# Performance work log

Hardware: AMD Instinct MI355X
Metric: run time of the kernel (lower is better)

## Reference

```python
import jax, jax.numpy as jnp
import numpy as np
import math

SIDE = 48          # image height = width (positions = SIDE*SIDE)
WIN = 3            # window_size (odd, image mode)
K = WIN * WIN      # neighbor_count
FD = 32            # field_dim
HID = 64           # hidden_dim
NH = 4             # num_hypotheses
RD = 8             # relative_dim
JOINT = 3 * FD + RD
CLIP = 3.0
TEMP = 1.0
GATE_EPS = 1e-6
ETA = 1.0          # warmup_eta


def _neighbor_windows(x, side, win):
    B = x.shape[0]
    rest = x.shape[2:]
    g = x.reshape((B, side, side) + rest)
    p = win // 2
    gp = jnp.pad(g, [(0, 0), (p, p), (p, p)] + [(0, 0)] * len(rest))
    w = jnp.stack([gp[:, dy:dy + side, dx:dx + side]
                   for dy in range(win) for dx in range(win)], axis=3)
    return w.reshape((B, side * side, win * win) + rest)


def _mlp(x, w1, b1, w2, b2):
    # Linear -> GELU (exact, like torch nn.GELU()) -> Linear, squeeze last dim
    return (jax.nn.gelu(x @ w1 + b1, approximate=False) @ w2 + b2)[..., 0]


def setup_inputs() -> dict:
    key = jax.random.key(0)
    ks = jax.random.split(key, 16)
    B, P = 2, SIDE * SIDE
    inp = {
        'hypothesis_state': jax.random.normal(ks[0], (B, P, NH, FD), jnp.float32),
        'activation': jax.random.uniform(ks[1], (B, P, NH), jnp.float32),
        'drive': jax.random.uniform(ks[2], (B, P, NH), jnp.float32),
        'resistance': jax.random.uniform(ks[3], (B, P, NH), jnp.float32),
        'relative': 0.02 * jax.random.normal(ks[4], (K, RD), jnp.float32),
        'ln_w': jnp.ones((JOINT,), jnp.float32),
        'ln_b': jnp.zeros((JOINT,), jnp.float32),
        'sup_w1': jax.random.normal(ks[5], (JOINT, HID), jnp.float32) / math.sqrt(JOINT),
        'sup_b1': jnp.zeros((HID,), jnp.float32),
        'sup_w2': jax.random.normal(ks[6], (HID, 1), jnp.float32) / math.sqrt(HID),
        'sup_b2': jnp.zeros((1,), jnp.float32),
        'con_w1': jax.random.normal(ks[7], (JOINT, HID), jnp.float32) / math.sqrt(JOINT),
        'con_b1': jnp.zeros((HID,), jnp.float32),
        'con_w2': jax.random.normal(ks[8], (HID, 1), jnp.float32) / math.sqrt(HID),
        'con_b2': jnp.zeros((1,), jnp.float32),
        'eml_bias': jnp.float32(-0.1),
    }
    return inp


def reference(hypothesis_state, activation, drive, resistance, relative,
              ln_w, ln_b, sup_w1, sup_b1, sup_w2, sup_b2,
              con_w1, con_b1, con_w2, con_b2, eml_bias):
    B, P, H, D = hypothesis_state.shape
    side = int(math.isqrt(P))
    # windowed neighbor gather (image mode, zero-padded 3x3)
    sw = _neighbor_windows(hypothesis_state, side, WIN)   # [B,P,K,H,D]
    aw = _neighbor_windows(activation, side, WIN)          # [B,P,K,H]
    valid = _neighbor_windows(jnp.ones((1, P), hypothesis_state.dtype), side, WIN)  # [1,P,K]

    shp = (B, P, H, K, H)
    tgt = jnp.broadcast_to(hypothesis_state[:, :, :, None, None, :], shp + (D,))
    src = jnp.broadcast_to(sw[:, :, None, :, :, :], shp + (D,))
    rel = jnp.broadcast_to(relative[None, None, None, :, None, :], shp + (RD,))
    joint = jnp.concatenate([tgt, src, tgt - src, rel], axis=-1)  # [B,P,H,K,H,JOINT]
    mu = joint.mean(-1, keepdims=True)
    var = joint.var(-1, keepdims=True)
    joint = (joint - mu) * jax.lax.rsqrt(var + 1e-5) * ln_w + ln_b

    support_value = jax.nn.softplus(_mlp(joint, sup_w1, sup_b1, sup_w2, sup_b2))  # [B,P,H,K,H]
    conflict_value = jax.nn.softplus(_mlp(joint, con_w1, con_b1, con_w2, con_b2))

    gate = aw[:, :, None, :, :] * valid[:, :, None, :, None]   # [B,P,1,K,H]
    gate_mass = jnp.maximum(gate.sum((3, 4)), GATE_EPS)        # [B,P,1]
    support = (support_value * gate).sum((3, 4)) / gate_mass   # [B,P,H]
    conflict = (conflict_value * gate).sum((3, 4)) / gate_mass

    pdrive = drive + support
    presist = resistance + conflict
    # EMLUnit(dim=1, clip_value, init_bias=-0.1): clipped warmup-scaled drive/resistance balance
    energy = jnp.clip(ETA * (pdrive - presist) + eml_bias, -CLIP, CLIP)
    # EMLActivationBudget(temperature)
    act = jax.nn.sigmoid(energy / TEMP)
    budget_loss = act.mean()
    entropy = -(act * jnp.log(act + 1e-8) + (1.0 - act) * jnp.log(1.0 - act + 1e-8)).mean()
    active_rate = (act > 0.5).astype(jnp.float32).mean()

    return (support, conflict, pdrive, presist, energy, act,
            jnp.broadcast_to(gate_mass, support.shape), budget_loss, entropy, active_rate)
```

## Files before the change

### kernel.cpp

```cpp
#include <hip/hip_runtime.h>
#include <hip/hip_bf16.h>
#include <math.h>

#define SIDE 48
#define PPOS (SIDE*SIDE)
#define NBATCH 2
#define NHYP 4
#define FD 32
#define RD 8
#define NJ 104
#define NBP (NBATCH*PPOS)
#define NOUT (NBP*NHYP)
#define THREADS 512
#define NROWS 576
#define NBLK (NBP/4)
#define WS_SR   16
#define WS_SQR  28
#define WS_SC   40
#define WS_RC   64
#define WS_S    1216
#define WS_T    1344
#define WS_W2   1472
#define WS_WBF  1600
#define WS_WAF  3648
#define WS_PART 5696

typedef __attribute__((ext_vector_type(8))) short short8;
typedef __attribute__((ext_vector_type(4))) float f32x4;
typedef __attribute__((ext_vector_type(2))) float f32x2;
union U8 { uint4 u4; short8 s8; };

__device__ __forceinline__ float bflo(unsigned u) { return __uint_as_float(u << 16); }
__device__ __forceinline__ float bfhi(unsigned u) { return __uint_as_float(u & 0xffff0000u); }
__device__ __forceinline__ unsigned packbf2(float a, float b) {
    unsigned ua = __float_as_uint(a), ub = __float_as_uint(b);
    unsigned ra = (ua + 0x7fffu + ((ua >> 16) & 1u)) >> 16;
    unsigned rb = (ub + 0x7fffu + ((ub >> 16) & 1u)) & 0xffff0000u;
    return ra | rb;
}
__device__ __forceinline__ float softplusf(float v) {
    return fmaxf(v, 0.f) + log1pf(expf(-fabsf(v)));
}

#define W1X(kk, j) ((j) < 64 ? sup_w1[(kk)*64 + (j)] : con_w1[(kk)*64 + (j) - 64])

__global__ __launch_bounds__(512) void eml_fold(
    const float* __restrict__ rel, const float* __restrict__ ln_w, const float* __restrict__ ln_b,
    const float* __restrict__ sup_w1, const float* __restrict__ sup_b1,
    const float* __restrict__ sup_w2, const float* __restrict__ sup_b2,
    const float* __restrict__ con_w1, const float* __restrict__ con_b1,
    const float* __restrict__ con_w2, const float* __restrict__ con_b2,
    const float* __restrict__ eml_bias, float* __restrict__ ws)
{
    const int tid = threadIdx.x;
    const int bid = blockIdx.x;
    unsigned* wsd = reinterpret_cast<unsigned*>(ws);
    __shared__ float pS[4][128], pT[4][128];

    if (bid < 8) {
        int u = bid*512 + tid;
        int sel = u >> 11, v2 = u & 2047;
        int n = v2 >> 8, l = (v2 >> 2) & 63, j = v2 & 3;
        int k0 = (l >> 4)*8 + 2*j, col = n*16 + (l & 15);
        float lo, hi;
        if (sel == 0) {
            lo = ln_w[32+k0]*W1X(32+k0,col)     - ln_w[64+k0]*W1X(64+k0,col);
            hi = ln_w[32+k0+1]*W1X(32+k0+1,col) - ln_w[64+k0+1]*W1X(64+k0+1,col);
        } else {
            lo = ln_w[k0]*W1X(k0,col)     + ln_w[64+k0]*W1X(64+k0,col);
            hi = ln_w[k0+1]*W1X(k0+1,col) + ln_w[64+k0+1]*W1X(64+k0+1,col);
        }
        wsd[(sel ? WS_WAF : WS_WBF) + v2] = packbf2(lo, hi);
    } else if (bid == 8) {
        #pragma unroll
        for (int u0 = 0; u0 < 2; ++u0) {
            int u = u0*512 + tid;
            int k = u >> 7, j = u & 127;
            float a = 0.f;
            #pragma unroll
            for (int i = 0; i < 8; ++i) a += rel[k*8+i] * ln_w[96+i] * W1X(96+i, j);
            ws[WS_RC + u] = a;
        }
    } else if (bid == 9) {
        if (tid < 128) {
            int u = 1024 + tid;
            int k = u >> 7, j = u & 127;
            float a = 0.f;
            #pragma unroll
            for (int i = 0; i < 8; ++i) a += rel[k*8+i] * ln_w[96+i] * W1X(96+i, j);
            ws[WS_RC + u] = a;
        } else if (tid < 137) {
            int kk = tid - 128;
            float s = 0.f, sq = 0.f;
            #pragma unroll
            for (int i = 0; i < 8; ++i) { float v = rel[kk*8+i]; s += v; sq += v*v; }
            ws[WS_SR+kk] = s; ws[WS_SQR+kk] = sq;
        } else if (tid == 140) {
            ws[WS_SC] = sup_b2[0]; ws[WS_SC+1] = con_b2[0]; ws[WS_SC+2] = eml_bias[0];
        }
    } else {
        int col = tid & 127, seg = tid >> 7;
        float S = 0.f, T = 0.f;
        for (int kk = seg*26; kk < seg*26 + 26; ++kk) {
            float w = W1X(kk, col);
            S += ln_w[kk]*w; T += ln_b[kk]*w;
        }
        pS[seg][col] = S; pT[seg][col] = T;
        __syncthreads();
        if (tid < 128) {
            float Tt = pT[0][tid] + pT[1][tid] + pT[2][tid] + pT[3][tid]
                       + (tid < 64 ? sup_b1[tid] : con_b1[tid-64]);
            ws[WS_S + tid]  = pS[0][tid] + pS[1][tid] + pS[2][tid] + pS[3][tid];
            ws[WS_T + tid]  = Tt * 32.f + 512.5f;
            ws[WS_W2 + tid] = (tid < 64 ? sup_w2[tid] : con_w2[tid-64]);
        }
    }
}

__global__ __launch_bounds__(THREADS, 8) void eml_main(
    const float* __restrict__ hs, const float* __restrict__ act_in,
    const float* __restrict__ drive, const float* __restrict__ resist,
    float* __restrict__ out, const float* __restrict__ cst,
    float* __restrict__ part)
{
    __shared__ __align__(16) unsigned sB[64*68];
    __shared__ __align__(16) float    sA[16*132];
    __shared__ union __align__(16) UU {
        __hip_bfloat16 snb[64*40];
        unsigned svcv[NROWS];
    } u;
    __shared__ __align__(16) float sdot[64*16];
    __shared__ __align__(16) float sgelu[1024];
    __shared__ float sact[64], sSt[64], sSq[64];
    __shared__ float sSr[9], sSqr[9];

    const int tid = threadIdx.x;
    const int blk = blockIdx.x;
    const int b   = blk / 576;
    const int rm  = blk % 576;
    const int y0  = (rm / 24) * 2;
    const int x0  = (rm % 24) * 2;

    #pragma unroll
    for (int i = tid; i < 1024; i += THREADS) {
        float x = (float)(i - 512) * 0.03125f;
        sgelu[i] = 0.5f * x * (1.0f + erff(x * 0.70710678118654752f));
    }

    const int vec = tid >> 3, q = tid & 7;
    const int nb1 = vec >> 2, h1 = vec & 3;
    const int yy = y0 + (nb1 >> 2) - 1, xx = x0 + (nb1 & 3) - 1;
    const bool vld = (yy >= 0) && (yy < SIDE) && (xx >= 0) && (xx < SIDE);
    const int npos = b*PPOS + yy*SIDE + xx;
    float4 v = make_float4(0.f, 0.f, 0.f, 0.f);
    if (vld) v = *reinterpret_cast<const float4*>(&hs[((size_t)npos*NHYP + h1)*FD + q*4]);
    {
        unsigned* drow = reinterpret_cast<unsigned*>(&u.snb[vec*40]);
        drow[q*2]   = packbf2(v.x, v.y);
        drow[q*2+1] = packbf2(v.z, v.w);
        float s  = v.x + v.y + v.z + v.w;
        float sq = v.x*v.x + v.y*v.y + v.z*v.z + v.w*v.w;
        s += __shfl_xor(s, 1); sq += __shfl_xor(sq, 1);
        s += __shfl_xor(s, 2); sq += __shfl_xor(sq, 2);
        s += __shfl_xor(s, 4); sq += __shfl_xor(sq, 4);
        if (q == 0) {
            sSt[vec] = s; sSq[vec] = sq;
            sact[vec] = vld ? act_in[npos*NHYP + h1] : 0.f;
        }
    }
    if (tid < 9) { sSr[tid] = cst[WS_SR+tid]; sSqr[tid] = cst[WS_SQR+tid]; }
    __syncthreads();

    {
        const int wv = tid >> 6, lane = tid & 63;
        const int fr = lane & 15, fq = lane >> 4;
        const char* snbB = reinterpret_cast<const char*>(u.snb);
        U8 bB, bA;
        bB.u4 = reinterpret_cast<const uint4*>(cst + WS_WBF)[wv*64 + lane];
        bA.u4 = reinterpret_cast<const uint4*>(cst + WS_WAF)[wv*64 + lane];
        #pragma unroll
        for (int m = 0; m < 4; ++m) {
            U8 a; a.u4 = *reinterpret_cast<const uint4*>(snbB + (m*16 + fr)*80 + fq*16);
            f32x4 acc = {0.f, 0.f, 0.f, 0.f};
            acc = __builtin_amdgcn_mfma_f32_16x16x32_bf16(a.s8, bB.s8, acc, 0, 0, 0);
            #pragma unroll
            for (int j = 0; j < 4; ++j) {
                float o = __shfl_xor(acc[j], 1);
                if (!(lane & 1))
                    sB[(m*16 + fq*4 + j)*68 + wv*8 + (fr >> 1)] = packbf2(acc[j], o);
            }
        }
        const int trow = (fr < 8) ? (20 + fr) : (28 + fr);
        U8 at; at.u4 = *reinterpret_cast<const uint4*>(snbB + trow*80 + fq*16);
        {
            f32x4 acc = {0.f, 0.f, 0.f, 0.f};
            acc = __builtin_amdgcn_mfma_f32_16x16x32_bf16(at.s8, bA.s8, acc, 0, 0, 0);
            #pragma unroll
            for (int j = 0; j < 4; ++j)
                sA[(fq*4 + j)*132 + wv*16 + fr] = acc[j];
        }
        if (wv < 4) {
            U8 s2; s2.u4 = *reinterpret_cast<const uint4*>(snbB + (wv*16 + fr)*80 + fq*16);
            f32x4 acc = {0.f, 0.f, 0.f, 0.f};
            acc = __builtin_amdgcn_mfma_f32_16x16x32_bf16(at.s8, s2.s8, acc, 0, 0, 0);
            *reinterpret_cast<f32x4*>(&sdot[(wv*16 + fr)*16 + fq*4]) = acc;
        }
    }
    __syncthreads();

    for (int ri = tid; ri < NROWS; ri += THREADS) {
        const int pos = ri / 144, r = ri % 144;
        const int hh = r / 36, s = r % 36, k = s >> 2, h2 = s & 3;
        const int nbr  = ((pos >> 1) + k/3)*4 + ((pos & 1) + k%3);
        const int srow = nbr*4 + h2;
        const float gate = sact[srow];
        float svv = 0.f, cvv = 0.f;
        if (gate > 0.f) {
            const int cidx = pos*4 + hh;
            const int crow = (pos < 2 ? 20 : 28) + cidx;
            const float dot = sdot[srow*16 + cidx];
            const float mu   = (2.f*sSt[crow] + sSr[k]) * (1.f/NJ);
            const float ssum = 2.f*sSq[crow] + 2.f*sSq[srow] - 2.f*dot + sSqr[k];
            const float rinv = rsqrtf(ssum*(1.f/NJ) - mu*mu + 1e-5f);
            const float r32  = rinv * 32.f;
            const float b32  = -mu * r32;
            const f32x2 r32_2 = {r32, r32};
            const f32x2 b32_2 = {b32, b32};
            const float* aR  = &sA[cidx*132];
            const uint4* bR  = reinterpret_cast<const uint4*>(&sB[srow*68]);
            const float* rck = cst + WS_RC + k*128;
            const f32x2* S2  = reinterpret_cast<const f32x2*>(cst + WS_S);
            const f32x2* T2  = reinterpret_cast<const f32x2*>(cst + WS_T);
            float outs = 0.f, outc = 0.f;
            #pragma unroll 2
            for (int jq = 0; jq < 16; ++jq) {
                uint4 ub = bR[jq];
                const f32x2* a2 = reinterpret_cast<const f32x2*>(aR + jq*8);
                const f32x2* c2 = reinterpret_cast<const f32x2*>(rck + jq*8);
                float accv = 0.f;
                #define PAIR(UW, P) { \
                    f32x2 bv; bv.x = bflo(UW); bv.y = bfhi(UW); \
                    f32x2 d  = a2[P] + bv + c2[P]; \
                    f32x2 qv = r32_2*d + (b32_2*S2[jq*4+P] + T2[jq*4+P]); \
                    float g0 = sgelu[(unsigned)qv.x]; \
                    float g1 = sgelu[(unsigned)qv.y]; \
                    accv = fmaf(g0, cst[WS_W2 + jq*8 + 2*(P)], accv); \
                    accv = fmaf(g1, cst[WS_W2 + jq*8 + 2*(P) + 1], accv); }
                PAIR(ub.x, 0)
                PAIR(ub.y, 1)
                PAIR(ub.z, 2)
                PAIR(ub.w, 3)
                #undef PAIR
                if (jq < 8) outs += accv; else outc += accv;
            }
            svv = softplusf(outs + cst[WS_SC]);
            cvv = softplusf(outc + cst[WS_SC+1]);
        }
        u.svcv[ri] = packbf2(svv*gate, cvv*gate);
    }
    __syncthreads();

    if (tid < 64) {
        const int pos4 = tid >> 4, hh4 = (tid >> 2) & 3, qq = tid & 3;
        float svs = 0.f, cvs = 0.f, mass = 0.f;
        #pragma unroll
        for (int i = 0; i < 9; ++i) {
            int s = qq*9 + i;
            unsigned pp = u.svcv[pos4*144 + hh4*36 + s];
            svs += bflo(pp); cvs += bfhi(pp);
            int kk = s >> 2, h2 = s & 3;
            int nbr = ((pos4 >> 1) + kk/3)*4 + ((pos4 & 1) + kk%3);
            mass += sact[nbr*4 + h2];
        }
        svs += __shfl_xor(svs, 1); cvs += __shfl_xor(cvs, 1); mass += __shfl_xor(mass, 1);
        svs += __shfl_xor(svs, 2); cvs += __shfl_xor(cvs, 2); mass += __shfl_xor(mass, 2);
        float bl = 0.f, en = 0.f, ar = 0.f;
        if (qq == 0) {
            mass = fmaxf(mass, 1e-6f);
            const float support  = svs / mass;
            const float conflict = cvs / mass;
            const int bph = (b*PPOS + (y0 + (pos4 >> 1))*SIDE + x0 + (pos4 & 1))*NHYP + hh4;
            const float pd = drive[bph]  + support;
            const float pr = resist[bph] + conflict;
            float e = fminf(fmaxf(pd - pr + cst[WS_SC+2], -3.f), 3.f);
            const float a = 1.f / (1.f + expf(-e));
            out[0*NOUT + bph] = support;
            out[1*NOUT + bph] = conflict;
            out[2*NOUT + bph] = pd;
            out[3*NOUT + bph] = pr;
            out[4*NOUT + bph] = e;
            out[5*NOUT + bph] = a;
            out[6*NOUT + bph] = mass;
            bl = a;
            en = -(a*logf(a + 1e-8f) + (1.f - a)*logf(1.f - a + 1e-8f));
            ar = (a > 0.5f) ? 1.f : 0.f;
        }
        #pragma unroll
        for (int off = 32; off > 0; off >>= 1) {
            bl += __shfl_down(bl, off); en += __shfl_down(en, off); ar += __shfl_down(ar, off);
        }
        if (tid == 0) {
            part[blk]          = bl;
            part[NBLK + blk]   = en;
            part[2*NBLK + blk] = ar;
        }
    }
}

__global__ __launch_bounds__(256) void eml_final(const float* __restrict__ part, float* __restrict__ out3)
{
    __shared__ float red[4*3];
    float bl = 0.f, en = 0.f, ar = 0.f;
    for (int i = threadIdx.x; i < NBLK; i += 256) {
        bl += part[i];
        en += part[NBLK + i];
        ar += part[2*NBLK + i];
    }
    #pragma unroll
    for (int off = 32; off > 0; off >>= 1) {
        bl += __shfl_down(bl, off); en += __shfl_down(en, off); ar += __shfl_down(ar, off);
    }
    const int lane = threadIdx.x & 63, wid = threadIdx.x >> 6;
    if (lane == 0) { red[wid*3] = bl; red[wid*3+1] = en; red[wid*3+2] = ar; }
    __syncthreads();
    if (threadIdx.x == 0) {
        float b2 = 0.f, e2 = 0.f, a2 = 0.f;
        for (int w = 0; w < 4; ++w) { b2 += red[w*3]; e2 += red[w*3+1]; a2 += red[w*3+2]; }
        const float inv = 1.0f / (float)NOUT;
        out3[0] = b2*inv; out3[1] = e2*inv; out3[2] = a2*inv;
    }
}

extern "C" void kernel_launch(void* const* d_in, const int* in_sizes, int n_in,
                              void* d_out, int out_size, void* d_ws, size_t ws_size,
                              hipStream_t stream)
{
    (void)in_sizes; (void)n_in; (void)out_size; (void)ws_size;
    const float* hs    = (const float*)d_in[0];
    const float* act   = (const float*)d_in[1];
    const float* drv   = (const float*)d_in[2];
    const float* res   = (const float*)d_in[3];
    const float* rel   = (const float*)d_in[4];
    const float* lnw   = (const float*)d_in[5];
    const float* lnb   = (const float*)d_in[6];
    const float* sw1   = (const float*)d_in[7];
    const float* sb1   = (const float*)d_in[8];
    const float* sw2   = (const float*)d_in[9];
    const float* sb2   = (const float*)d_in[10];
    const float* cw1   = (const float*)d_in[11];
    const float* cb1   = (const float*)d_in[12];
    const float* cw2   = (const float*)d_in[13];
    const float* cb2   = (const float*)d_in[14];
    const float* ebias = (const float*)d_in[15];
    float* out = (float*)d_out;
    float* ws  = (float*)d_ws;

    eml_fold<<<dim3(11), dim3(512), 0, stream>>>(
        rel, lnw, lnb, sw1, sb1, sw2, sb2, cw1, cb1, cw2, cb2, ebias, ws);
    eml_main<<<dim3(NBLK), dim3(THREADS), 0, stream>>>(
        hs, act, drv, res, out, ws, ws + WS_PART);
    eml_final<<<dim3(1), dim3(256), 0, stream>>>(ws + WS_PART, out + 7*NOUT);
}
```

Baseline: 47.64 us.

## Enlarge per-block tile from 2x2 to 2x3 positions to cut halo overhead

Each block now handles a 2x3 patch of output positions, so it loads a 4x5 neighbor halo instead of 2x2 positions with a 4x4 halo. Each loaded neighbor row feeds more outputs, and the grid shrinks from 1152 to 768 blocks. The MFMA tiles for the projections and dot products are reorganised around the 24 center rows, and the final partial reduction now spans two waves through shared memory. In exchange, shared memory per block grows, the occupancy hint drops from 8 to 6, and some MFMA lanes do padded work.

```diff
diff --git a/kernel.cpp b/kernel.cpp
--- a/kernel.cpp
+++ b/kernel.cpp
@@ -12,8 +12,8 @@
 #define NBP (NBATCH*PPOS)
 #define NOUT (NBP*NHYP)
 #define THREADS 512
-#define NROWS 576
-#define NBLK (NBP/4)
+#define NROWS 864
+#define NBLK 768
 #define WS_SR   16
 #define WS_SQR  28
 #define WS_SC   40
@@ -117,29 +117,29 @@
     }
 }
 
-__global__ __launch_bounds__(THREADS, 8) void eml_main(
+__global__ __launch_bounds__(THREADS, 6) void eml_main(
     const float* __restrict__ hs, const float* __restrict__ act_in,
     const float* __restrict__ drive, const float* __restrict__ resist,
     float* __restrict__ out, const float* __restrict__ cst,
     float* __restrict__ part)
 {
-    __shared__ __align__(16) unsigned sB[64*68];
-    __shared__ __align__(16) float    sA[16*132];
+    __shared__ __align__(16) unsigned sB[80*68];
+    __shared__ __align__(16) float    sA[24*132];
     __shared__ union __align__(16) UU {
-        __hip_bfloat16 snb[64*40];
+        __hip_bfloat16 snb[80*40];
         unsigned svcv[NROWS];
     } u;
-    __shared__ __align__(16) float sdot[64*16];
+    __shared__ __align__(16) float sdot[80*24];
     __shared__ __align__(16) float sgelu[1024];
-    __shared__ float sact[64], sSt[64], sSq[64];
+    __shared__ float sact[80], sSt[80], sSq[80];
     __shared__ float sSr[9], sSqr[9];
 
     const int tid = threadIdx.x;
     const int blk = blockIdx.x;
-    const int b   = blk / 576;
-    const int rm  = blk % 576;
-    const int y0  = (rm / 24) * 2;
-    const int x0  = (rm % 24) * 2;
+    const int b   = blk / 384;
+    const int rm  = blk % 384;
+    const int y0  = (rm / 16) * 2;
+    const int x0  = (rm % 16) * 3;
 
     #pragma unroll
     for (int i = tid; i < 1024; i += THREADS) {
@@ -147,22 +147,28 @@
         sgelu[i] = 0.5f * x * (1.0f + erff(x * 0.70710678118654752f));
     }
 
-    const int vec = tid >> 3, q = tid & 7;
-    const int nb1 = vec >> 2, h1 = vec & 3;
-    const int yy = y0 + (nb1 >> 2) - 1, xx = x0 + (nb1 & 3) - 1;
-    const bool vld = (yy >= 0) && (yy < SIDE) && (xx >= 0) && (xx < SIDE);
-    const int npos = b*PPOS + yy*SIDE + xx;
-    float4 v = make_float4(0.f, 0.f, 0.f, 0.f);
-    if (vld) v = *reinterpret_cast<const float4*>(&hs[((size_t)npos*NHYP + h1)*FD + q*4]);
-    {
+    if (tid < 320) {
+        const int vec = tid >> 2, q = tid & 3;
+        const int nb1 = vec >> 2, h1 = vec & 3;
+        const int ny = nb1 / 5, nx = nb1 % 5;
+        const int yy = y0 + ny - 1, xx = x0 + nx - 1;
+        const bool vld = (yy >= 0) && (yy < SIDE) && (xx >= 0) && (xx < SIDE);
+        const int npos = b*PPOS + yy*SIDE + xx;
+        float4 v0 = make_float4(0.f,0.f,0.f,0.f), v1 = make_float4(0.f,0.f,0.f,0.f);
+        if (vld) {
+            const float4* p = reinterpret_cast<const float4*>(&hs[((size_t)npos*NHYP + h1)*FD + q*8]);
+            v0 = p[0]; v1 = p[1];
+        }
         unsigned* drow = reinterpret_cast<unsigned*>(&u.snb[vec*40]);
-        drow[q*2]   = packbf2(v.x, v.y);
-        drow[q*2+1] = packbf2(v.z, v.w);
-        float s  = v.x + v.y + v.z + v.w;
-        float sq = v.x*v.x + v.y*v.y + v.z*v.z + v.w*v.w;
+        drow[q*4+0] = packbf2(v0.x, v0.y);
+        drow[q*4+1] = packbf2(v0.z, v0.w);
+        drow[q*4+2] = packbf2(v1.x, v1.y);
+        drow[q*4+3] = packbf2(v1.z, v1.w);
+        float s  = (v0.x+v0.y+v0.z+v0.w) + (v1.x+v1.y+v1.z+v1.w);
+        float sq = (v0.x*v0.x+v0.y*v0.y+v0.z*v0.z+v0.w*v0.w)
+                 + (v1.x*v1.x+v1.y*v1.y+v1.z*v1.z+v1.w*v1.w);
         s += __shfl_xor(s, 1); sq += __shfl_xor(sq, 1);
         s += __shfl_xor(s, 2); sq += __shfl_xor(sq, 2);
-        s += __shfl_xor(s, 4); sq += __shfl_xor(sq, 4);
         if (q == 0) {
             sSt[vec] = s; sSq[vec] = sq;
             sact[vec] = vld ? act_in[npos*NHYP + h1] : 0.f;
@@ -179,7 +185,7 @@
         bB.u4 = reinterpret_cast<const uint4*>(cst + WS_WBF)[wv*64 + lane];
         bA.u4 = reinterpret_cast<const uint4*>(cst + WS_WAF)[wv*64 + lane];
         #pragma unroll
-        for (int m = 0; m < 4; ++m) {
+        for (int m = 0; m < 5; ++m) {
             U8 a; a.u4 = *reinterpret_cast<const uint4*>(snbB + (m*16 + fr)*80 + fq*16);
             f32x4 acc = {0.f, 0.f, 0.f, 0.f};
             acc = __builtin_amdgcn_mfma_f32_16x16x32_bf16(a.s8, bB.s8, acc, 0, 0, 0);
@@ -190,20 +196,44 @@
                     sB[(m*16 + fq*4 + j)*68 + wv*8 + (fr >> 1)] = packbf2(acc[j], o);
             }
         }
-        const int trow = (fr < 8) ? (20 + fr) : (28 + fr);
-        U8 at; at.u4 = *reinterpret_cast<const uint4*>(snbB + trow*80 + fq*16);
+        const int pos0 = fr >> 2, hh0 = fr & 3;
+        const int trow0 = ((pos0/3 + 1)*5 + (pos0%3) + 1)*4 + hh0;
+        int trow1 = 0;
+        if (fr < 8) {
+            const int t1 = 16 + fr, pos1 = t1 >> 2, hh1 = t1 & 3;
+            trow1 = ((pos1/3 + 1)*5 + (pos1%3) + 1)*4 + hh1;
+        }
+        U8 at0, at1;
+        at0.u4 = *reinterpret_cast<const uint4*>(snbB + trow0*80 + fq*16);
+        at1.u4 = *reinterpret_cast<const uint4*>(snbB + trow1*80 + fq*16);
         {
             f32x4 acc = {0.f, 0.f, 0.f, 0.f};
-            acc = __builtin_amdgcn_mfma_f32_16x16x32_bf16(at.s8, bA.s8, acc, 0, 0, 0);
+            acc = __builtin_amdgcn_mfma_f32_16x16x32_bf16(at0.s8, bA.s8, acc, 0, 0, 0);
             #pragma unroll
             for (int j = 0; j < 4; ++j)
                 sA[(fq*4 + j)*132 + wv*16 + fr] = acc[j];
         }
-        if (wv < 4) {
-            U8 s2; s2.u4 = *reinterpret_cast<const uint4*>(snbB + (wv*16 + fr)*80 + fq*16);
+        {
             f32x4 acc = {0.f, 0.f, 0.f, 0.f};
-            acc = __builtin_amdgcn_mfma_f32_16x16x32_bf16(at.s8, s2.s8, acc, 0, 0, 0);
-            *reinterpret_cast<f32x4*>(&sdot[(wv*16 + fr)*16 + fq*4]) = acc;
+            acc = __builtin_amdgcn_mfma_f32_16x16x32_bf16(at1.s8, bA.s8, acc, 0, 0, 0);
+            if (fq < 2) {
+                #pragma unroll
+                for (int j = 0; j < 4; ++j)
+                    sA[(16 + fq*4 + j)*132 + wv*16 + fr] = acc[j];
+            }
+        }
+        #pragma unroll
+        for (int pass = 0; pass < 2; ++pass) {
+            int uu = pass ? (8 + wv) : wv;
+            if (pass && wv >= 2) break;
+            const int mt = uu / 5, n = uu % 5;
+            U8 sfr; sfr.u4 = *reinterpret_cast<const uint4*>(snbB + (n*16 + fr)*80 + fq*16);
+            f32x4 acc = {0.f, 0.f, 0.f, 0.f};
+            acc = __builtin_amdgcn_mfma_f32_16x16x32_bf16(mt ? at1.s8 : at0.s8, sfr.s8, acc, 0, 0, 0);
+            if (!mt)
+                *reinterpret_cast<f32x4*>(&sdot[(n*16 + fr)*24 + fq*4]) = acc;
+            else if (fq < 2)
+                *reinterpret_cast<f32x4*>(&sdot[(n*16 + fr)*24 + 16 + fq*4]) = acc;
         }
     }
     __syncthreads();
@@ -211,14 +241,15 @@
     for (int ri = tid; ri < NROWS; ri += THREADS) {
         const int pos = ri / 144, r = ri % 144;
         const int hh = r / 36, s = r % 36, k = s >> 2, h2 = s & 3;
-        const int nbr  = ((pos >> 1) + k/3)*4 + ((pos & 1) + k%3);
+        const int py = pos / 3, px = pos % 3;
+        const int nbr  = (py + k/3)*5 + (px + k%3);
         const int srow = nbr*4 + h2;
         const float gate = sact[srow];
         float svv = 0.f, cvv = 0.f;
         if (gate > 0.f) {
             const int cidx = pos*4 + hh;
-            const int crow = (pos < 2 ? 20 : 28) + cidx;
-            const float dot = sdot[srow*16 + cidx];
+            const int crow = ((py + 1)*5 + px + 1)*4 + hh;
+            const float dot = sdot[srow*24 + cidx];
             const float mu   = (2.f*sSt[crow] + sSr[k]) * (1.f/NJ);
             const float ssum = 2.f*sSq[crow] + 2.f*sSq[srow] - 2.f*dot + sSqr[k];
             const float rinv = rsqrtf(ssum*(1.f/NJ) - mu*mu + 1e-5f);
@@ -260,8 +291,11 @@
     }
     __syncthreads();
 
-    if (tid < 64) {
-        const int pos4 = tid >> 4, hh4 = (tid >> 2) & 3, qq = tid & 3;
+    float bl = 0.f, en = 0.f, ar = 0.f;
+    if (tid < 96) {
+        const int g = tid >> 2, qq = tid & 3;
+        const int pos4 = g >> 2, hh4 = g & 3;
+        const int py = pos4 / 3, px = pos4 % 3;
         float svs = 0.f, cvs = 0.f, mass = 0.f;
         #pragma unroll
         for (int i = 0; i < 9; ++i) {
@@ -269,17 +303,16 @@
             unsigned pp = u.svcv[pos4*144 + hh4*36 + s];
             svs += bflo(pp); cvs += bfhi(pp);
             int kk = s >> 2, h2 = s & 3;
-            int nbr = ((pos4 >> 1) + kk/3)*4 + ((pos4 & 1) + kk%3);
+            int nbr = (py + kk/3)*5 + (px + kk%3);
             mass += sact[nbr*4 + h2];
         }
         svs += __shfl_xor(svs, 1); cvs += __shfl_xor(cvs, 1); mass += __shfl_xor(mass, 1);
         svs += __shfl_xor(svs, 2); cvs += __shfl_xor(cvs, 2); mass += __shfl_xor(mass, 2);
-        float bl = 0.f, en = 0.f, ar = 0.f;
         if (qq == 0) {
             mass = fmaxf(mass, 1e-6f);
             const float support  = svs / mass;
             const float conflict = cvs / mass;
-            const int bph = (b*PPOS + (y0 + (pos4 >> 1))*SIDE + x0 + (pos4 & 1))*NHYP + hh4;
+            const int bph = (b*PPOS + (y0 + py)*SIDE + x0 + px)*NHYP + hh4;
             const float pd = drive[bph]  + support;
             const float pr = resist[bph] + conflict;
             float e = fminf(fmaxf(pd - pr + cst[WS_SC+2], -3.f), 3.f);
@@ -295,15 +328,23 @@
             en = -(a*logf(a + 1e-8f) + (1.f - a)*logf(1.f - a + 1e-8f));
             ar = (a > 0.5f) ? 1.f : 0.f;
         }
+    }
+    if (tid < 128) {
         #pragma unroll
         for (int off = 32; off > 0; off >>= 1) {
             bl += __shfl_down(bl, off); en += __shfl_down(en, off); ar += __shfl_down(ar, off);
         }
-        if (tid == 0) {
-            part[blk]          = bl;
-            part[NBLK + blk]   = en;
-            part[2*NBLK + blk] = ar;
-        }
+        if ((tid & 63) == 0) {
+            sdot[(tid >> 6)*4 + 0] = bl;
+            sdot[(tid >> 6)*4 + 1] = en;
+            sdot[(tid >> 6)*4 + 2] = ar;
+        }
+    }
+    __syncthreads();
+    if (tid == 0) {
+        part[blk]          = sdot[0] + sdot[4];
+        part[NBLK + blk]   = sdot[1] + sdot[5];
+        part[2*NBLK + blk] = sdot[2] + sdot[6];
     }
 }
 
```

New measurement: 44.59 us. 6.4% less time.
